# Performance work log

Measured on AMD Instinct MI355X. Metric: run time of the kernel, lower is better.

Reference implementation:

```python
import jax, jax.numpy as jnp
import numpy as np

IN, H, L, B, S = 512, 1024, 6, 64, 256


def setup_inputs() -> dict:
    key = jax.random.key(0)
    ks = jax.random.split(key, 8)
    stdv = 1.0 / np.sqrt(H)
    u = lambda k, shp: jax.random.uniform(k, shp, jnp.float32, -stdv, stdv)
    x = jax.random.normal(ks[0], (B, S, IN), jnp.float32)
    # gate order along last axis of 4H: i, f, c(g), o
    U0 = u(ks[1], (IN, 4 * H))   # layer 0 input weights
    V0 = u(ks[2], (H, 4 * H))    # layer 0 recurrent weights
    b0 = u(ks[3], (4 * H,))
    U = u(ks[4], (L - 1, H, 4 * H))  # layers 1..L-1 input weights
    V = u(ks[5], (L - 1, H, 4 * H))
    b = u(ks[6], (L - 1, 4 * H))
    return {"x": x, "U0": U0, "V0": V0, "b0": b0, "U": U, "V": V, "b": b}


def _cell(xt, h, c, Um, Vm, bm):
    # fused 4-gate GEMM: [B, in] @ [in, 4H] + [B, H] @ [H, 4H]
    z = xt @ Um + h @ Vm + bm
    i, f, g, o = jnp.split(z, 4, axis=-1)
    i = jax.nn.sigmoid(i)
    f = jax.nn.sigmoid(f)
    g = jnp.tanh(g)
    o = jax.nn.sigmoid(o)
    c = f * c + i * g
    h = o * jnp.tanh(c)
    return h, c


def reference(x, U0, V0, b0, U, V, b):
    # Dropout is identity in eval mode (faithful to module.eval()).
    Bb = x.shape[0]
    h0 = jnp.zeros((L, Bb, H), x.dtype)
    c0 = jnp.zeros((L, Bb, H), x.dtype)

    def step(carry, xt):
        h, c = carry
        hs, cs = [], []
        inp = xt
        hn, cn = _cell(inp, h[0], c[0], U0, V0, b0)
        hs.append(hn); cs.append(cn); inp = hn
        for l in range(L - 1):  # fixed small layer loop
            hn, cn = _cell(inp, h[l + 1], c[l + 1], U[l], V[l], b[l])
            hs.append(hn); cs.append(cn); inp = hn
        return (jnp.stack(hs), jnp.stack(cs)), inp

    (hf, cf), seq = jax.lax.scan(step, (h0, c0), jnp.swapaxes(x, 0, 1))
    hidden_seq = jnp.swapaxes(seq, 0, 1)  # [B, S, H]
    return hidden_seq, hf, cf
```

## Files before the change

kernel.cpp:

```cpp
#include <hip/hip_runtime.h>
#include <hip/hip_cooperative_groups.h>

#define B_ 64
#define H_ 1024
#define IN_ 512
#define S_ 256
#define L_ 6
#define NG_ 4096
#define NTASK 768
#define NTICK (S_ + L_ - 1)

typedef __bf16 bf16x8 __attribute__((ext_vector_type(8)));
typedef float f32x4 __attribute__((ext_vector_type(4)));
typedef float f32x2 __attribute__((ext_vector_type(2)));
typedef unsigned short ushort8v __attribute__((ext_vector_type(8)));
typedef unsigned short ushort_t;

#define WP_BYTES 96468992ul
#define XB_BYTES 16777216ul
#define HBF_ELEMS 786432ul
#define LSLOT 65536ul
#define XSLOT 32768ul

__host__ __device__ __forceinline__ size_t poff(int l, int jb) {
  return (l == 0) ? (size_t)jb * 49152ul
                  : 6291456ul + ((size_t)(l - 1) * 128 + jb) * 65536ul;
}

#define MFMA16(a, b, c) __builtin_amdgcn_mfma_f32_16x16x32_bf16(a, b, c, 0, 0, 0)
#define WAITN(n) asm volatile("s_waitcnt vmcnt(" #n ")" ::: "memory")
#define SB0() __builtin_amdgcn_sched_barrier(0)

__device__ __forceinline__ unsigned short f2bf(float f) {
  union { float f; unsigned u; } v; v.f = f;
  unsigned r = v.u + 0x7fffu + ((v.u >> 16) & 1u);
  return (unsigned short)(r >> 16);
}

__global__ void k_pack_w(const float* __restrict__ U0, const float* __restrict__ V0,
                         const float* __restrict__ U, const float* __restrict__ V,
                         ushort_t* __restrict__ Wp) {
  const int bx = blockIdx.x;
  const int l = bx >> 7, jb = bx & 127;
  ushort_t* __restrict__ panel = Wp + poff(l, jb);
  const int KU = (l == 0) ? IN_ : H_;
  const int NU = KU >> 6;
  const int NCH = NU + 16;
  const float* __restrict__ Usrc = (l == 0) ? U0 : U + (size_t)(l - 1) * H_ * NG_;
  const float* __restrict__ Vsrc = (l == 0) ? V0 : V + (size_t)(l - 1) * H_ * NG_;
  const int t = threadIdx.x, lane = t & 63, g4 = t >> 6;
  const int l15 = lane & 15, kg = lane >> 4;
  for (int p = 0; p < NCH; ++p) {
    const int gi = p * 4 + g4;
    const int c = gi >> 2, u = gi & 3, nf = u >> 1, ks = u & 1;
    const int n = (nf * 2 + (l15 >> 3)) * 1024 + jb * 8 + (l15 & 7);
    const int k = c * 64 + ks * 32 + kg * 8;
    const float* __restrict__ src =
        (c < NU) ? (Usrc + (size_t)k * NG_ + n)
                 : (Vsrc + (size_t)(k - KU) * NG_ + n);
    ushort8v uv;
#pragma unroll
    for (int e = 0; e < 8; ++e) uv[e] = f2bf(src[(size_t)e * NG_]);
    *(ushort8v*)(panel + (size_t)gi * 512 + lane * 8) = uv;
  }
}

__global__ void k_cvt_x(const float* __restrict__ x, ushort_t* __restrict__ xb) {
  const int tt = blockIdx.x;
  const int tid = threadIdx.x;
  const int b = tid >> 2, kq = (tid & 3) << 7;
  const float* __restrict__ src = x + ((size_t)b * S_ + tt) * IN_ + kq;
  ushort_t* __restrict__ dst = xb + (size_t)tt * XSLOT;
  const int m = b >> 4, l15 = b & 15;
#pragma unroll
  for (int kk = 0; kk < 128; kk += 8) {
    float4 v0 = *(const float4*)(src + kk);
    float4 v1 = *(const float4*)(src + kk + 4);
    ushort8v u = { f2bf(v0.x), f2bf(v0.y), f2bf(v0.z), f2bf(v0.w),
                   f2bf(v1.x), f2bf(v1.y), f2bf(v1.z), f2bf(v1.w) };
    const int k = kq + kk;
    const int c = k >> 6, ksl = (k >> 5) & 1, kg = (k & 31) >> 3;
    *(ushort8v*)(dst + (((size_t)c * 8 + m * 2 + ksl) * 64 + kg * 16 + l15) * 8) = u;
  }
}

template<int NCH>
__device__ __forceinline__ void gemm_q(f32x4 acc[4][2],
                                       const ushort_t* __restrict__ panel,
                                       const ushort_t* __restrict__ A1,
                                       const ushort_t* __restrict__ A2,
                                       int w, int lane) {
  constexpr int NU = NCH - 16;
  constexpr int Q = NCH / 4;
  bf16x8 Wb[2][4];
  bf16x8 Ab[2][8];
#define LDU(p) (*(const bf16x8*)(p))
#define ISSUE(c, bk) do { \
    const ushort_t* wp_ = panel + (size_t)(c) * 2048 + lane * 8; \
    Wb[bk][0] = LDU(wp_); \
    Wb[bk][1] = LDU(wp_ + 512); \
    Wb[bk][2] = LDU(wp_ + 1024); \
    Wb[bk][3] = LDU(wp_ + 1536); \
    const ushort_t* ap_ = ((c) < NU \
        ? A1 + (size_t)(c) * 4096 : A2 + (size_t)((c) - NU) * 4096) + lane * 8; \
    Ab[bk][0] = LDU(ap_); \
    Ab[bk][1] = LDU(ap_ + 512); \
    Ab[bk][2] = LDU(ap_ + 1024); \
    Ab[bk][3] = LDU(ap_ + 1536); \
    Ab[bk][4] = LDU(ap_ + 2048); \
    Ab[bk][5] = LDU(ap_ + 2560); \
    Ab[bk][6] = LDU(ap_ + 3072); \
    Ab[bk][7] = LDU(ap_ + 3584); \
  } while (0)
  const int c0 = w * Q;
  ISSUE(c0, 0);
  if (Q > 1) ISSUE(c0 + 1, 1);
  SB0();
#pragma unroll
  for (int j = 0; j < Q; ++j) {
    if (j + 1 < Q) { WAITN(12); } else { WAITN(0); }
    SB0();
    const int bk = j & 1;
#pragma unroll
    for (int ks = 0; ks < 2; ++ks)
#pragma unroll
      for (int m = 0; m < 4; ++m) {
        acc[m][0] = MFMA16(Ab[bk][m * 2 + ks], Wb[bk][ks], acc[m][0]);
        acc[m][1] = MFMA16(Ab[bk][m * 2 + ks], Wb[bk][2 + ks], acc[m][1]);
      }
    SB0();
    if (j + 2 < Q) ISSUE(c0 + j + 2, bk);
    SB0();
  }
#undef ISSUE
#undef LDU
}

__global__ void __launch_bounds__(256)
k_lstm(const ushort_t* __restrict__ xb,
       const ushort_t* __restrict__ Wp,
       const float* __restrict__ b0,
       const float* __restrict__ bL,
       ushort_t* __restrict__ hbf,
       float* __restrict__ out, int multi) {
  cooperative_groups::grid_group grid = cooperative_groups::this_grid();
  float* __restrict__ seq = out;
  float* __restrict__ hf = out + (size_t)B_ * S_ * H_;
  float* __restrict__ cf = hf + (size_t)L_ * B_ * H_;
  __shared__ float zsp[4][64][33];
  __shared__ float hstF[512];

  const int tid = threadIdx.x;
  const int w = tid >> 6;
  const int lane = tid & 63;
  const int l15 = lane & 15;
  const int kg = lane >> 4;
  const int wg = blockIdx.x;
  const int nwg = gridDim.x;

  const int grow = tid >> 2;
  const int gq = (tid & 3) << 1;
  float creg[2] = {0.f, 0.f};

  for (int T = 0; T < NTICK; ++T) {
    for (int task = wg; task < NTASK; task += nwg) {
      const int l = task >> 7;
      const int jb = task & 127;
      const int t = T - l;
      if (t < 0 || t >= S_) continue;
      const ushort_t* __restrict__ hprev = hbf + (size_t)((T + 1) & 1) * (L_ * LSLOT);
      ushort_t* __restrict__ hcur = hbf + (size_t)(T & 1) * (L_ * LSLOT) + (size_t)l * LSLOT;
      const ushort_t* __restrict__ panel = Wp + poff(l, jb);
      const ushort_t* __restrict__ A2 = hprev + (size_t)l * LSLOT;

      f32x4 acc[4][2];
#pragma unroll
      for (int m = 0; m < 4; ++m) {
        acc[m][0] = (f32x4){0.f, 0.f, 0.f, 0.f};
        acc[m][1] = (f32x4){0.f, 0.f, 0.f, 0.f};
      }
      if (l == 0)
        gemm_q<24>(acc, panel, xb + (size_t)t * XSLOT, A2, w, lane);
      else
        gemm_q<32>(acc, panel, hprev + (size_t)(l - 1) * LSLOT, A2, w, lane);

#pragma unroll
      for (int m = 0; m < 4; ++m)
#pragma unroll
        for (int nf = 0; nf < 2; ++nf)
#pragma unroll
          for (int j = 0; j < 4; ++j)
            zsp[w][m * 16 + kg * 4 + j][nf * 16 + l15] = acc[m][nf][j];
      __syncthreads();

      {
        const int hc0 = (jb << 3) + gq;
        const float* __restrict__ bias = (l == 0) ? b0 : (bL + (size_t)(l - 1) * NG_);
        const size_t cbase = ((size_t)l * B_ + grow) * H_ + hc0;
        f32x2 cold;
        if (multi) {
          if (t > 0) cold = *(const f32x2*)(cf + cbase);
          else cold = (f32x2){0.f, 0.f};
        } else {
          cold = (f32x2){creg[0], creg[1]};
        }
        f32x2 hv2, cn2;
#pragma unroll
        for (int q = 0; q < 2; ++q) {
          const int hcl = gq + q;
          float z[4];
#pragma unroll
          for (int g = 0; g < 4; ++g) {
            const int c32 = (g >> 1) * 16 + (g & 1) * 8 + hcl;
            z[g] = zsp[0][grow][c32] + zsp[1][grow][c32] +
                   zsp[2][grow][c32] + zsp[3][grow][c32] +
                   bias[g * 1024 + hc0 + q];
          }
          float iv = 1.f / (1.f + expf(-z[0]));
          float fv = 1.f / (1.f + expf(-z[1]));
          float gv = tanhf(z[2]);
          float ov = 1.f / (1.f + expf(-z[3]));
          float cn = fv * cold[q] + iv * gv;
          cn2[q] = cn;
          creg[q] = cn;
          float hv = ov * tanhf(cn);
          hv2[q] = hv;
          hstF[grow * 8 + hcl] = hv;
        }
        if (multi || t == S_ - 1) *(f32x2*)(cf + cbase) = cn2;
        if (t == S_ - 1) *(f32x2*)(hf + cbase) = hv2;
        if (l == L_ - 1)
          *(f32x2*)(seq + ((size_t)grow * S_ + t) * H_ + hc0) = hv2;
      }
      __syncthreads();

      if (tid < 64) {
        const int m = tid >> 4, lr = tid & 15;
        const float* hp = &hstF[(m * 16 + lr) * 8];
        ushort8v u8 = { f2bf(hp[0]), f2bf(hp[1]), f2bf(hp[2]), f2bf(hp[3]),
                        f2bf(hp[4]), f2bf(hp[5]), f2bf(hp[6]), f2bf(hp[7]) };
        *(ushort8v*)(hcur +
                     (((size_t)(jb >> 3) * 8 + m * 2 + ((jb >> 2) & 1)) * 64 +
                      ((jb & 3) * 16 + lr)) * 8) = u8;
      }
      __syncthreads();
    }
    grid.sync();
  }
}

extern "C" void kernel_launch(void* const* d_in, const int* in_sizes, int n_in,
                              void* d_out, int out_size, void* d_ws, size_t ws_size,
                              hipStream_t stream) {
  const float* x = (const float*)d_in[0];
  const float* U0 = (const float*)d_in[1];
  const float* V0 = (const float*)d_in[2];
  const float* b0 = (const float*)d_in[3];
  const float* U = (const float*)d_in[4];
  const float* V = (const float*)d_in[5];
  const float* bL = (const float*)d_in[6];
  float* out = (float*)d_out;

  char* ws = (char*)d_ws;
  unsigned short* Wp = (unsigned short*)ws;
  unsigned short* xb = (unsigned short*)(ws + WP_BYTES);
  unsigned short* hbf = (unsigned short*)(ws + WP_BYTES + XB_BYTES);

  hipLaunchKernelGGL(k_pack_w, dim3(NTASK), dim3(256), 0, stream, U0, V0, U, V, Wp);
  hipLaunchKernelGGL(k_cvt_x, dim3(S_), dim3(256), 0, stream, x, xb);
  hipMemsetAsync(hbf, 0, HBF_ELEMS * 2, stream);

  int maxB = 0;
  hipOccupancyMaxActiveBlocksPerMultiprocessor(&maxB, k_lstm, 256, 0);
  int nwg = maxB * 256;
  if (nwg > NTASK) nwg = NTASK;
  if (nwg < 64) nwg = 64;
  int multi = (nwg < NTASK) ? 1 : 0;

  void* args[] = { (void*)&xb, (void*)&Wp, (void*)&b0, (void*)&bL,
                   (void*)&hbf, (void*)&out, (void*)&multi };
  hipError_t e = hipLaunchCooperativeKernel((void*)k_lstm, dim3(nwg), dim3(256),
                                            args, 0, stream);
  if (e != hipSuccess) {
    (void)hipGetLastError();
    nwg = 256; multi = 1;
    void* args2[] = { (void*)&xb, (void*)&Wp, (void*)&b0, (void*)&bL,
                      (void*)&hbf, (void*)&out, (void*)&multi };
    hipLaunchCooperativeKernel((void*)k_lstm, dim3(nwg), dim3(256),
                               args2, 0, stream);
  }
}
```

Before: 13.56 ms.

## Replace cooperative grid.sync with hierarchical per-XCD atomic tree barrier

Swaps the cooperative-groups grid barrier for a custom two-level barrier. Blocks first count in per-XCD counters (blockIdx&7), and the last arrival per XCD bumps a global counter that releases per-XCD generation flags. Waiters spin with s_sleep. This targets the cost of the 261 grid-wide barriers in the persistent LSTM wavefront. It also adds launch_bounds min 3 blocks/SM, which may raise occupancy or cause register spills, and it relies on nwg being divisible by 8 with blocks evenly distributed across XCDs.

```diff
diff --git a/kernel.cpp b/kernel.cpp
--- a/kernel.cpp
+++ b/kernel.cpp
@@ -18,7 +18,7 @@
 
 #define WP_BYTES 96468992ul
 #define XB_BYTES 16777216ul
-#define HBF_ELEMS 786432ul
+#define HBF_BYTES 1572864ul
 #define LSLOT 65536ul
 #define XSLOT 32768ul
 
@@ -35,6 +35,34 @@
   union { float f; unsigned u; } v; v.f = f;
   unsigned r = v.u + 0x7fffu + ((v.u >> 16) & 1u);
   return (unsigned short)(r >> 16);
+}
+
+__device__ __forceinline__ void tree_sync(int* __restrict__ bar, int gen, int nloc) {
+  __syncthreads();
+  if (threadIdx.x == 0) {
+    __threadfence();
+    const int xcd = blockIdx.x & 7;
+    int a = __hip_atomic_fetch_add(&bar[xcd * 32], 1, __ATOMIC_ACQ_REL,
+                                   __HIP_MEMORY_SCOPE_AGENT);
+    if (a == nloc - 1) {
+      __hip_atomic_store(&bar[xcd * 32], 0, __ATOMIC_RELAXED,
+                         __HIP_MEMORY_SCOPE_AGENT);
+      int r = __hip_atomic_fetch_add(&bar[256], 1, __ATOMIC_ACQ_REL,
+                                     __HIP_MEMORY_SCOPE_AGENT);
+      if (r == 7) {
+        __hip_atomic_store(&bar[256], 0, __ATOMIC_RELAXED,
+                           __HIP_MEMORY_SCOPE_AGENT);
+#pragma unroll
+        for (int i = 0; i < 8; ++i)
+          __hip_atomic_store(&bar[512 + i * 32], gen, __ATOMIC_RELEASE,
+                             __HIP_MEMORY_SCOPE_AGENT);
+      }
+    }
+    while (__hip_atomic_load(&bar[512 + (blockIdx.x & 7) * 32], __ATOMIC_ACQUIRE,
+                             __HIP_MEMORY_SCOPE_AGENT) < gen)
+      __builtin_amdgcn_s_sleep(1);
+  }
+  __syncthreads();
 }
 
 __global__ void k_pack_w(const float* __restrict__ U0, const float* __restrict__ V0,
@@ -136,14 +164,14 @@
 #undef LDU
 }
 
-__global__ void __launch_bounds__(256)
+__global__ void __launch_bounds__(256, 3)
 k_lstm(const ushort_t* __restrict__ xb,
        const ushort_t* __restrict__ Wp,
        const float* __restrict__ b0,
        const float* __restrict__ bL,
        ushort_t* __restrict__ hbf,
+       int* __restrict__ bar,
        float* __restrict__ out, int multi) {
-  cooperative_groups::grid_group grid = cooperative_groups::this_grid();
   float* __restrict__ seq = out;
   float* __restrict__ hf = out + (size_t)B_ * S_ * H_;
   float* __restrict__ cf = hf + (size_t)L_ * B_ * H_;
@@ -157,6 +185,7 @@
   const int kg = lane >> 4;
   const int wg = blockIdx.x;
   const int nwg = gridDim.x;
+  const int nloc = nwg >> 3;
 
   const int grow = tid >> 2;
   const int gq = (tid & 3) << 1;
@@ -245,7 +274,7 @@
       }
       __syncthreads();
     }
-    grid.sync();
+    tree_sync(bar, T + 1, nloc);
   }
 }
 
@@ -265,10 +294,12 @@
   unsigned short* Wp = (unsigned short*)ws;
   unsigned short* xb = (unsigned short*)(ws + WP_BYTES);
   unsigned short* hbf = (unsigned short*)(ws + WP_BYTES + XB_BYTES);
+  int* bar = (int*)(ws + WP_BYTES + XB_BYTES + HBF_BYTES);
 
   hipLaunchKernelGGL(k_pack_w, dim3(NTASK), dim3(256), 0, stream, U0, V0, U, V, Wp);
   hipLaunchKernelGGL(k_cvt_x, dim3(S_), dim3(256), 0, stream, x, xb);
-  hipMemsetAsync(hbf, 0, HBF_ELEMS * 2, stream);
+  hipMemsetAsync(hbf, 0, HBF_BYTES, stream);
+  hipMemsetAsync(bar, 0, 4096, stream);
 
   int maxB = 0;
   hipOccupancyMaxActiveBlocksPerMultiprocessor(&maxB, k_lstm, 256, 0);
@@ -278,14 +309,14 @@
   int multi = (nwg < NTASK) ? 1 : 0;
 
   void* args[] = { (void*)&xb, (void*)&Wp, (void*)&b0, (void*)&bL,
-                   (void*)&hbf, (void*)&out, (void*)&multi };
+                   (void*)&hbf, (void*)&bar, (void*)&out, (void*)&multi };
   hipError_t e = hipLaunchCooperativeKernel((void*)k_lstm, dim3(nwg), dim3(256),
                                             args, 0, stream);
   if (e != hipSuccess) {
     (void)hipGetLastError();
     nwg = 256; multi = 1;
     void* args2[] = { (void*)&xb, (void*)&Wp, (void*)&b0, (void*)&bL,
-                      (void*)&hbf, (void*)&out, (void*)&multi };
+                      (void*)&hbf, (void*)&bar, (void*)&out, (void*)&multi };
     hipLaunchCooperativeKernel((void*)k_lstm, dim3(nwg), dim3(256),
                                args2, 0, stream);
   }
```

After: 19.39 ms. +43.0%, slower.
